# Performance work log

Measured on AMD Instinct MI355X. Metric: run time of the kernel, lower is better.

Reference implementation:

```python
import jax, jax.numpy as jnp
import numpy as np
from jax import lax

N_NEURONS = 2500
K = 50
T = 60
F = 5
H = 128
GROUP_SIZES = [800, 700, 600, 400]  # support_resistance, trend, pattern, volume
GID = jnp.asarray(np.repeat(np.arange(4), GROUP_SIZES))  # [N] specialty id per neuron
_BOUNDS = np.cumsum([0] + GROUP_SIZES)


def _lstm_layer(x, w_ih, w_hh, b_ih, b_hh):
    # x: [B,T,in]; PyTorch gate order i,f,g,o in the 4H weight rows
    B = x.shape[0]
    Hd = w_hh.shape[1]
    def step(carry, xt):
        h, c = carry
        g = xt @ w_ih.T + h @ w_hh.T + b_ih + b_hh
        i, f, gg, o = jnp.split(g, 4, axis=-1)
        c = jax.nn.sigmoid(f) * c + jax.nn.sigmoid(i) * jnp.tanh(gg)
        h = jax.nn.sigmoid(o) * jnp.tanh(c)
        return (h, c), h
    init = (jnp.zeros((B, Hd), x.dtype), jnp.zeros((B, Hd), x.dtype))
    (h, _), ys = lax.scan(step, init, jnp.swapaxes(x, 0, 1))
    return jnp.swapaxes(ys, 0, 1), h


def _forward(x, w_ih0, w_hh0, b_ih0, b_hh0, w_ih1, w_hh1, b_ih1, b_hh1,
             pw1, pb1, pw2, pb2, conn_w, sens, thr,
             iw1, ib1, iw2, ib2, iw3, ib3,
             hw_trend, hb_trend, hw_pat, hb_pat, hw_key, hb_key,
             hw_vol, hb_vol, hw_conf, hb_conf, conn_idx):
    seq, _ = _lstm_layer(x, w_ih0, w_hh0, b_ih0, b_hh0)
    _, h2 = _lstm_layer(seq, w_ih1, w_hh1, b_ih1, b_hh1)  # hidden[-1]: [B,H]
    # feature_projection: Linear->ReLU->Linear->Tanh
    base = jnp.tanh(jax.nn.relu(h2 @ pw1.T + pb1) @ pw2.T + pb2)  # [B,32]
    # broadcast base features to a per-neuron activation vector [B,N]
    reps = -(-N_NEURONS // base.shape[1])
    all_act = jnp.tile(base, (1, reps))[:, :N_NEURONS]
    # batched sparse gather + per-neuron weighted sum
    gathered = all_act[:, conn_idx]                       # [B,N,K]
    z = jnp.einsum('bnk,nk->bn', gathered, conn_w) * sens  # [B,N]
    # specialty-conditioned activation
    a = jnp.where(GID == 0, jax.nn.sigmoid(z - thr),
        jnp.where(GID == 1, jnp.tanh(z),
        jnp.where(GID == 2, jax.nn.relu(z - thr), jax.nn.sigmoid(z))))
    # integrator (dropout is eval-mode no-op)
    integ = jnp.tanh(jax.nn.relu(jax.nn.relu(a @ iw1.T + ib1) @ iw2.T + ib2) @ iw3.T + ib3)
    trend = integ @ hw_trend.T + hb_trend      # [B,3]
    pat = integ @ hw_pat.T + hb_pat            # [B,6]
    key_l = integ @ hw_key.T + hb_key          # [B,4]
    vol = integ @ hw_vol.T + hb_vol            # [B,1]
    conf = integ @ hw_conf.T + hb_conf         # [B,1]
    overall = jax.nn.sigmoid(conf)             # [B,1]
    means = jnp.stack([a[:, _BOUNDS[i]:_BOUNDS[i + 1]].mean(axis=1) for i in range(4)], axis=1)
    return jnp.concatenate([trend, pat, key_l, vol, conf, overall, means], axis=1)  # [B,20]


def setup_inputs() -> dict:
    key = jax.random.key(0)
    ks = iter(jax.random.split(key, 64))
    def rn(shape, s=0.05):
        return jax.random.normal(next(ks), shape, jnp.float32) * s
    B = 1024
    return {
        'x': jax.random.normal(next(ks), (B, T, F), jnp.float32),
        'conn_idx': jax.random.randint(next(ks), (N_NEURONS, K), 0, N_NEURONS, jnp.int32),
        'w_ih0': rn((4 * H, F)), 'w_hh0': rn((4 * H, H)),
        'b_ih0': rn((4 * H,), 0.01), 'b_hh0': rn((4 * H,), 0.01),
        'w_ih1': rn((4 * H, H)), 'w_hh1': rn((4 * H, H)),
        'b_ih1': rn((4 * H,), 0.01), 'b_hh1': rn((4 * H,), 0.01),
        'pw1': rn((64, H)), 'pb1': rn((64,), 0.01),
        'pw2': rn((32, 64)), 'pb2': rn((32,), 0.01),
        'conn_w': rn((N_NEURONS, K), 0.1),
        'sens': rn((N_NEURONS,), 0.1) + 1.0,
        'thr': rn((N_NEURONS,), 0.1) + 0.6,
        'iw1': rn((256, N_NEURONS), 0.01), 'ib1': rn((256,), 0.01),
        'iw2': rn((64, 256)), 'ib2': rn((64,), 0.01),
        'iw3': rn((32, 64)), 'ib3': rn((32,), 0.01),
        'hw_trend': rn((3, 32)), 'hb_trend': rn((3,), 0.01),
        'hw_pat': rn((6, 32)), 'hb_pat': rn((6,), 0.01),
        'hw_key': rn((4, 32)), 'hb_key': rn((4,), 0.01),
        'hw_vol': rn((1, 32)), 'hb_vol': rn((1,), 0.01),
        'hw_conf': rn((1, 32)), 'hb_conf': rn((1,), 0.01),
    }


def reference(x, conn_idx, w_ih0, w_hh0, b_ih0, b_hh0, w_ih1, w_hh1, b_ih1, b_hh1,
              pw1, pb1, pw2, pb2, conn_w, sens, thr,
              iw1, ib1, iw2, ib2, iw3, ib3,
              hw_trend, hb_trend, hw_pat, hb_pat, hw_key, hb_key,
              hw_vol, hb_vol, hw_conf, hb_conf):
    return _forward(x, w_ih0, w_hh0, b_ih0, b_hh0, w_ih1, w_hh1, b_ih1, b_hh1,
                    pw1, pb1, pw2, pb2, conn_w, sens, thr,
                    iw1, ib1, iw2, ib2, iw3, ib3,
                    hw_trend, hb_trend, hw_pat, hb_pat, hw_key, hb_key,
                    hw_vol, hb_vol, hw_conf, hb_conf, conn_idx)
```

## Files before the change

### kernel.cpp

```cpp
#include <hip/hip_runtime.h>
#include <hip/hip_bf16.h>
#include <math.h>

#define DEV __device__ __forceinline__

typedef short short8 __attribute__((ext_vector_type(8)));
typedef float f32x4  __attribute__((ext_vector_type(4)));

DEV float sigf(float x)   { return 1.0f / (1.0f + __expf(-x)); }
DEV float tanhft(float x) { return 1.0f - 2.0f / (__expf(2.0f * x) + 1.0f); }

DEV unsigned short f2bf(float f) {
    unsigned int u = __float_as_uint(f);
    unsigned int r = (u + 0x7FFFu + ((u >> 16) & 1u)) >> 16;
    return (unsigned short)r;
}
DEV float bf2f(unsigned short u) {
    return __uint_as_float(((unsigned int)u) << 16);
}

DEV void bar_lds() {
    asm volatile("s_waitcnt lgkmcnt(0)" ::: "memory");
    __builtin_amdgcn_s_barrier();
}

__global__ __launch_bounds__(256) void prep_kernel(
    const float* __restrict__ w_hh0, const float* __restrict__ w_ih1,
    const float* __restrict__ w_hh1,
    const float* __restrict__ b_ih0, const float* __restrict__ b_hh0,
    const float* __restrict__ b_ih1, const float* __restrict__ b_hh1,
    unsigned short* __restrict__ whh0h, unsigned short* __restrict__ wih1h,
    unsigned short* __restrict__ whh1h,
    float* __restrict__ bias0, float* __restrict__ bias1)
{
    int i = blockIdx.x * 256 + threadIdx.x;
    if (i < 65536) {
        whh0h[i] = f2bf(w_hh0[i]);
        wih1h[i] = f2bf(w_ih1[i]);
        whh1h[i] = f2bf(w_hh1[i]);
    } else if (i < 66048) {
        int c = i - 65536;
        bias0[c] = b_ih0[c] + b_hh0[c];
        bias1[c] = b_ih1[c] + b_hh1[c];
    }
}

__global__ __launch_bounds__(256) void prep_iw1_kernel(
    const float* __restrict__ iw1, unsigned short* __restrict__ iw1b)
{
    int i = blockIdx.x * 256 + threadIdx.x;
    if (i < 256 * 2528) {
        int row = i / 2528, k = i - row * 2528;
        iw1b[i] = (k < 2500) ? f2bf(iw1[row * 2500 + k]) : (unsigned short)0;
    }
}

__global__ __launch_bounds__(512, 2) void lstm_kernel(
    const float* __restrict__ x,
    const unsigned short* __restrict__ whh0,
    const unsigned short* __restrict__ wih1,
    const unsigned short* __restrict__ whh1,
    const float* __restrict__ wih0,
    const float* __restrict__ bias0, const float* __restrict__ bias1,
    float* __restrict__ h2out)
{
    __shared__ __align__(16) float          xs[4][304];
    __shared__ __align__(16) unsigned short h0s[2][16][136];
    __shared__ __align__(16) unsigned short h1s[2][16][136];
    __shared__ __align__(16) float          wsc[8][4][16][4];
    __shared__ float wih0s[2560];

    const int tid = threadIdx.x;
    const int b0  = blockIdx.x * 4;
    const int l15 = tid & 15;
    const int q   = (tid >> 4) & 3;
    const int w   = tid >> 6;
    const int j   = w * 16 + l15;
    const int q8  = q * 8;

    for (int i = tid; i < 1200; i += 512) {
        int m = i / 300, kk = i - m * 300;
        xs[m][kk] = x[(b0 + m) * 300 + kk];
    }
    for (int i = tid; i < 2560; i += 512) wih0s[i] = wih0[i];
    for (int i = tid; i < 2176; i += 512) {
        ((unsigned int*)h0s)[i] = 0u;
        ((unsigned int*)h1s)[i] = 0u;
    }

    float ub0[4], ub1[4];
#pragma unroll
    for (int g = 0; g < 4; ++g) {
        ub0[g] = bias0[g * 128 + j];
        ub1[g] = bias1[g * 128 + j];
    }

    short8 bh0[4][4], b1i[4][4];
#pragma unroll
    for (int g = 0; g < 4; ++g)
#pragma unroll
        for (int kc = 0; kc < 4; ++kc) {
            int off = (g * 128 + j) * 128 + kc * 32 + q8;
            bh0[g][kc] = *(const short8*)(whh0 + off);
            b1i[g][kc] = *(const short8*)(wih1 + off);
        }

    float c0 = 0.f, c1 = 0.f, hl = 0.f;
    __syncthreads();

    const unsigned short* wsb = whh1 + j * 128 + q8;

    for (int t = 0; t < 60; ++t) {
        const int p = t & 1;

        short8 wsv[4][4];
#pragma unroll
        for (int g = 0; g < 4; ++g) {
            wsv[g][0] = *(const short8*)(wsb + g * 16384);
            wsv[g][1] = *(const short8*)(wsb + g * 16384 + 32);
        }

        f32x4 acc[4];
#pragma unroll
        for (int g = 0; g < 4; ++g) acc[g] = (f32x4){0.f, 0.f, 0.f, 0.f};
        short8 af[4];
#pragma unroll
        for (int kc = 0; kc < 4; ++kc)
            af[kc] = *(const short8*)&h0s[p][l15][kc * 32 + q8];
#pragma unroll
        for (int kc = 0; kc < 4; ++kc)
#pragma unroll
            for (int g = 0; g < 4; ++g)
                acc[g] = __builtin_amdgcn_mfma_f32_16x16x32_bf16(af[kc], bh0[g][kc], acc[g], 0, 0, 0);

#pragma unroll
        for (int g = 0; g < 4; ++g) {
            wsv[g][2] = *(const short8*)(wsb + g * 16384 + 64);
            wsv[g][3] = *(const short8*)(wsb + g * 16384 + 96);
        }

        if (q == 0) {
#pragma unroll
            for (int g = 0; g < 4; ++g)
                *(f32x4*)&wsc[w][g][l15][0] = acc[g];
        }
        {
            const float* xr = &xs[q][t * 5];
            float x0 = xr[0], x1 = xr[1], x2 = xr[2], x3 = xr[3], x4 = xr[4];
            float gv[4];
#pragma unroll
            for (int g = 0; g < 4; ++g) {
                const float* wr = &wih0s[(g * 128 + j) * 5];
                float s = wsc[w][g][l15][q] + ub0[g];
                s = fmaf(x0, wr[0], s);
                s = fmaf(x1, wr[1], s);
                s = fmaf(x2, wr[2], s);
                s = fmaf(x3, wr[3], s);
                gv[g] = fmaf(x4, wr[4], s);
            }
            c0 = sigf(gv[1]) * c0 + sigf(gv[0]) * tanhft(gv[2]);
            float h = sigf(gv[3]) * tanhft(c0);
            h0s[1 - p][q][j] = f2bf(h);
        }

        bar_lds();

#pragma unroll
        for (int g = 0; g < 4; ++g) acc[g] = (f32x4){0.f, 0.f, 0.f, 0.f};
#pragma unroll
        for (int kc = 0; kc < 4; ++kc)
            af[kc] = *(const short8*)&h0s[1 - p][l15][kc * 32 + q8];
#pragma unroll
        for (int kc = 0; kc < 4; ++kc)
#pragma unroll
            for (int g = 0; g < 4; ++g)
                acc[g] = __builtin_amdgcn_mfma_f32_16x16x32_bf16(af[kc], b1i[g][kc], acc[g], 0, 0, 0);
#pragma unroll
        for (int kc = 0; kc < 4; ++kc)
            af[kc] = *(const short8*)&h1s[p][l15][kc * 32 + q8];
#pragma unroll
        for (int kc = 0; kc < 4; ++kc)
#pragma unroll
            for (int g = 0; g < 4; ++g)
                acc[g] = __builtin_amdgcn_mfma_f32_16x16x32_bf16(af[kc], wsv[g][kc], acc[g], 0, 0, 0);

        if (q == 0) {
#pragma unroll
            for (int g = 0; g < 4; ++g)
                *(f32x4*)&wsc[w][g][l15][0] = acc[g];
        }
        {
            float gv[4];
#pragma unroll
            for (int g = 0; g < 4; ++g)
                gv[g] = wsc[w][g][l15][q] + ub1[g];
            c1 = sigf(gv[1]) * c1 + sigf(gv[0]) * tanhft(gv[2]);
            float h = sigf(gv[3]) * tanhft(c1);
            h1s[1 - p][q][j] = f2bf(h);
            hl = h;
        }
    }

    h2out[(b0 + q) * 128 + j] = hl;
}

__global__ __launch_bounds__(256) void phase2_kernel(
    const float* __restrict__ h2, const float* __restrict__ pw1,
    const float* __restrict__ pb1, const float* __restrict__ pw2,
    const float* __restrict__ pb2, float* __restrict__ base)
{
    __shared__ float pw1s[64 * 129];
    __shared__ float pw2s[32 * 65];
    __shared__ float hs[4][128];
    __shared__ float p1s[4][64];

    const int tid = threadIdx.x;
    const int b0  = blockIdx.x * 4;

    for (int i = tid; i < 8192; i += 256) {
        int u = i >> 7, k = i & 127;
        pw1s[u * 129 + k] = pw1[i];
    }
    for (int i = tid; i < 2048; i += 256) {
        int u = i >> 6, k = i & 63;
        pw2s[u * 65 + k] = pw2[i];
    }
    for (int i = tid; i < 512; i += 256)
        hs[i >> 7][i & 127] = h2[b0 * 128 + i];
    __syncthreads();

    {
        const int r = tid >> 6, u = tid & 63;
        float acc = pb1[u];
        const float* wr = &pw1s[u * 129];
        const float* hr = &hs[r][0];
#pragma unroll 4
        for (int k = 0; k < 128; ++k) acc = fmaf(hr[k], wr[k], acc);
        p1s[r][u] = fmaxf(acc, 0.f);
    }
    __syncthreads();

    if (tid < 128) {
        const int r = tid >> 5, u2 = tid & 31;
        float a2 = pb2[u2];
        const float* wr = &pw2s[u2 * 65];
        const float* pr = &p1s[r][0];
#pragma unroll 4
        for (int k = 0; k < 64; ++k) a2 = fmaf(pr[k], wr[k], a2);
        base[(b0 + r) * 32 + u2] = tanhft(a2);
    }
}

__global__ __launch_bounds__(128) void weff_kernel(
    const int* __restrict__ conn_idx, const float* __restrict__ conn_w,
    float* __restrict__ weffT)
{
    __shared__ float s[128 * 33];
    int tid = threadIdx.x;
    int n = blockIdx.x * 128 + tid;
    float* sr = &s[tid * 33];
#pragma unroll
    for (int j = 0; j < 32; ++j) sr[j] = 0.f;
    if (n < 2500) {
        for (int k = 0; k < 50; ++k) {
            int idx = conn_idx[n * 50 + k];
            sr[idx & 31] += conn_w[n * 50 + k];
        }
        for (int j = 0; j < 32; ++j) weffT[j * 2500 + n] = sr[j];
    }
}

__global__ __launch_bounds__(256) void za_kernel(
    const float* __restrict__ base, const float* __restrict__ weffT,
    const float* __restrict__ sens, const float* __restrict__ thr,
    unsigned short* __restrict__ amat)
{
    __shared__ float bs[16][32];
    int tid = threadIdx.x;
    int bb = blockIdx.x / 10, nb = blockIdx.x % 10;
    int n = nb * 256 + tid;
    bool nv = n < 2500;
    bool pv = n < 2528;
    int nn = nv ? n : 0;
    for (int i = tid; i < 512; i += 256) bs[i >> 5][i & 31] = base[bb * 512 + i];
    __syncthreads();
    float w[32];
#pragma unroll
    for (int j = 0; j < 32; ++j) w[j] = weffT[j * 2500 + nn];
    float sn = sens[nn], tn = thr[nn];
    int g = (n < 800) ? 0 : (n < 1500) ? 1 : (n < 2100) ? 2 : 3;
#pragma unroll 2
    for (int r = 0; r < 16; ++r) {
        float z = 0.f;
#pragma unroll
        for (int j = 0; j < 32; ++j) z = fmaf(bs[r][j], w[j], z);
        z *= sn;
        float av;
        if (g == 0)      av = sigf(z - tn);
        else if (g == 1) av = tanhft(z);
        else if (g == 2) av = fmaxf(z - tn, 0.f);
        else             av = sigf(z);
        if (nv)      amat[(bb * 16 + r) * 2528 + n] = f2bf(av);
        else if (pv) amat[(bb * 16 + r) * 2528 + n] = 0;
    }
}

__global__ __launch_bounds__(128) void gemm_iw1_kernel(
    const unsigned short* __restrict__ ab, const unsigned short* __restrict__ wb,
    const float* __restrict__ ib1, float* __restrict__ t1)
{
    const int tid = threadIdx.x;
    const int wv  = tid >> 6;
    const int l15 = tid & 15, q = (tid >> 4) & 3, q8 = q * 8;
    const int row0 = blockIdx.y * 32 + wv * 16;
    const int col0 = blockIdx.x * 32;

    const unsigned short* A = ab + (row0 + l15) * 2528 + q8;
    const unsigned short* B = wb + (col0 + l15) * 2528 + q8;

    short8 a = *(const short8*)A;
    short8 b[2];
#pragma unroll
    for (int nt = 0; nt < 2; ++nt) b[nt] = *(const short8*)(B + nt * 16 * 2528);

    f32x4 acc[2];
#pragma unroll
    for (int nt = 0; nt < 2; ++nt) acc[nt] = (f32x4){0.f, 0.f, 0.f, 0.f};

    for (int c = 0; c < 79; ++c) {
        int cn = (c < 78) ? c + 1 : 78;
        short8 an = *(const short8*)(A + cn * 32);
        short8 bn[2];
#pragma unroll
        for (int nt = 0; nt < 2; ++nt)
            bn[nt] = *(const short8*)(B + nt * 16 * 2528 + cn * 32);
#pragma unroll
        for (int nt = 0; nt < 2; ++nt)
            acc[nt] = __builtin_amdgcn_mfma_f32_16x16x32_bf16(a, b[nt], acc[nt], 0, 0, 0);
        a = an;
#pragma unroll
        for (int nt = 0; nt < 2; ++nt) b[nt] = bn[nt];
    }

#pragma unroll
    for (int nt = 0; nt < 2; ++nt) {
        int n = col0 + nt * 16 + l15;
        float bias = ib1[n];
#pragma unroll
        for (int i = 0; i < 4; ++i) {
            int row = row0 + q * 4 + i;
            t1[row * 256 + n] = fmaxf(acc[nt][i] + bias, 0.f);
        }
    }
}

__global__ __launch_bounds__(256) void final_kernel(
    const float* __restrict__ t1, const float* __restrict__ iw2,
    const float* __restrict__ ib2, const float* __restrict__ iw3,
    const float* __restrict__ ib3,
    const float* __restrict__ hw_trend, const float* __restrict__ hb_trend,
    const float* __restrict__ hw_pat,   const float* __restrict__ hb_pat,
    const float* __restrict__ hw_key,   const float* __restrict__ hb_key,
    const float* __restrict__ hw_vol,   const float* __restrict__ hb_vol,
    const float* __restrict__ hw_conf,  const float* __restrict__ hb_conf,
    float* __restrict__ out)
{
    __shared__ float iw2s[64 * 257];
    __shared__ float iw3s[32 * 65];
    __shared__ float t1s[4][256];
    __shared__ float t2s[4][64];
    __shared__ float igs[4][32];

    const int tid = threadIdx.x;
    const int b0  = blockIdx.x * 4;

    for (int i = tid; i < 16384; i += 256) {
        int u = i >> 8, k = i & 255;
        iw2s[u * 257 + k] = iw2[i];
    }
    for (int i = tid; i < 2048; i += 256) {
        int u = i >> 6, k = i & 63;
        iw3s[u * 65 + k] = iw3[i];
    }
    for (int i = tid; i < 1024; i += 256)
        t1s[i >> 8][i & 255] = t1[b0 * 256 + i];
    __syncthreads();

    {
        const int r = tid >> 6, u = tid & 63;
        float acc = ib2[u];
        const float* wr = &iw2s[u * 257];
        const float* tr = &t1s[r][0];
#pragma unroll 4
        for (int k = 0; k < 256; ++k) acc = fmaf(tr[k], wr[k], acc);
        t2s[r][u] = fmaxf(acc, 0.f);
    }
    __syncthreads();

    if (tid < 128) {
        const int r = tid >> 5, u2 = tid & 31;
        float a2 = ib3[u2];
        const float* wr = &iw3s[u2 * 65];
        const float* tr = &t2s[r][0];
#pragma unroll 4
        for (int k = 0; k < 64; ++k) a2 = fmaf(tr[k], wr[k], a2);
        igs[r][u2] = tanhft(a2);
    }
    __syncthreads();

    if (tid < 60) {
        const int r = tid / 15, t15 = tid % 15;
        const int b = b0 + r;
        const float* w; const float* bb; int j, off;
        if (t15 < 3)        { w = hw_trend; bb = hb_trend; j = t15;     off = 0; }
        else if (t15 < 9)   { w = hw_pat;   bb = hb_pat;   j = t15 - 3; off = 3; }
        else if (t15 < 13)  { w = hw_key;   bb = hb_key;   j = t15 - 9; off = 9; }
        else if (t15 == 13) { w = hw_vol;   bb = hb_vol;   j = 0;       off = 13; }
        else                { w = hw_conf;  bb = hb_conf;  j = 0;       off = 14; }
        float a3 = bb[j];
#pragma unroll
        for (int k = 0; k < 32; ++k) a3 = fmaf(igs[r][k], w[j * 32 + k], a3);
        out[b * 20 + off + j] = a3;
        if (t15 == 14) out[b * 20 + 15] = sigf(a3);
    }
}

__global__ __launch_bounds__(256) void means_kernel(
    const unsigned short* __restrict__ amat, float* __restrict__ out)
{
    __shared__ float red[16];
    int b = blockIdx.x, tid = threadIdx.x;
    float parts[4] = {0.f, 0.f, 0.f, 0.f};
    for (int n0 = tid * 8; n0 < 2500; n0 += 2048) {
        short8 v = *(const short8*)(amat + b * 2528 + n0);
#pragma unroll
        for (int e = 0; e < 8; ++e) {
            int n = n0 + e;
            float f = bf2f((unsigned short)v[e]);
            if (n < 800)       parts[0] += f;
            else if (n < 1500) parts[1] += f;
            else if (n < 2100) parts[2] += f;
            else               parts[3] += f;
        }
    }
    int lane = tid & 63, wv = tid >> 6;
#pragma unroll
    for (int g = 0; g < 4; ++g) {
        float v = parts[g];
        for (int s = 32; s > 0; s >>= 1) v += __shfl_down(v, s, 64);
        if (lane == 0) red[wv * 4 + g] = v;
    }
    __syncthreads();
    if (tid < 4) {
        float s = red[tid] + red[4 + tid] + red[8 + tid] + red[12 + tid];
        float invg = (tid == 0) ? (1.f / 800.f) : (tid == 1) ? (1.f / 700.f)
                   : (tid == 2) ? (1.f / 600.f) : (1.f / 400.f);
        out[b * 20 + 16 + tid] = s * invg;
    }
}

extern "C" void kernel_launch(void* const* d_in, const int* in_sizes, int n_in,
                              void* d_out, int out_size, void* d_ws, size_t ws_size,
                              hipStream_t stream)
{
    const float* x        = (const float*)d_in[0];
    const int*   conn_idx = (const int*)  d_in[1];
    const float* w_ih0    = (const float*)d_in[2];
    const float* w_hh0    = (const float*)d_in[3];
    const float* b_ih0    = (const float*)d_in[4];
    const float* b_hh0    = (const float*)d_in[5];
    const float* w_ih1    = (const float*)d_in[6];
    const float* w_hh1    = (const float*)d_in[7];
    const float* b_ih1    = (const float*)d_in[8];
    const float* b_hh1    = (const float*)d_in[9];
    const float* pw1      = (const float*)d_in[10];
    const float* pb1      = (const float*)d_in[11];
    const float* pw2      = (const float*)d_in[12];
    const float* pb2      = (const float*)d_in[13];
    const float* conn_w   = (const float*)d_in[14];
    const float* sens     = (const float*)d_in[15];
    const float* thr      = (const float*)d_in[16];
    const float* iw1      = (const float*)d_in[17];
    const float* ib1      = (const float*)d_in[18];
    const float* iw2      = (const float*)d_in[19];
    const float* ib2      = (const float*)d_in[20];
    const float* iw3      = (const float*)d_in[21];
    const float* ib3      = (const float*)d_in[22];
    const float* hw_trend = (const float*)d_in[23];
    const float* hb_trend = (const float*)d_in[24];
    const float* hw_pat   = (const float*)d_in[25];
    const float* hb_pat   = (const float*)d_in[26];
    const float* hw_key   = (const float*)d_in[27];
    const float* hb_key   = (const float*)d_in[28];
    const float* hw_vol   = (const float*)d_in[29];
    const float* hb_vol   = (const float*)d_in[30];
    const float* hw_conf  = (const float*)d_in[31];
    const float* hb_conf  = (const float*)d_in[32];
    float* out = (float*)d_out;
    float* ws  = (float*)d_ws;

    unsigned short* whh0h = (unsigned short*)(ws);
    unsigned short* wih1h = (unsigned short*)(ws + 32768);
    unsigned short* whh1h = (unsigned short*)(ws + 65536);
    float* bias0  = ws + 98304;
    float* bias1  = ws + 98816;
    float* h2     = ws + 99328;
    float* base_  = ws + 230400;
    float* weffT  = ws + 263168;
    float* t1     = ws + 343168;
    unsigned short* iw1b   = (unsigned short*)(ws + 605312);
    unsigned short* amatbf = (unsigned short*)(ws + 928896);

    prep_kernel<<<258, 256, 0, stream>>>(w_hh0, w_ih1, w_hh1,
                                         b_ih0, b_hh0, b_ih1, b_hh1,
                                         whh0h, wih1h, whh1h, bias0, bias1);
    prep_iw1_kernel<<<2528, 256, 0, stream>>>(iw1, iw1b);
    lstm_kernel<<<256, 512, 0, stream>>>(x, whh0h, wih1h, whh1h, w_ih0,
                                         bias0, bias1, h2);
    phase2_kernel<<<256, 256, 0, stream>>>(h2, pw1, pb1, pw2, pb2, base_);
    weff_kernel<<<20, 128, 0, stream>>>(conn_idx, conn_w, weffT);
    za_kernel<<<640, 256, 0, stream>>>(base_, weffT, sens, thr, amatbf);
    gemm_iw1_kernel<<<dim3(8, 32), 128, 0, stream>>>(amatbf, iw1b, ib1, t1);
    final_kernel<<<256, 256, 0, stream>>>(t1, iw2, ib2, iw3, ib3,
                                          hw_trend, hb_trend, hw_pat, hb_pat,
                                          hw_key, hb_key, hw_vol, hb_vol,
                                          hw_conf, hb_conf, out);
    means_kernel<<<1024, 256, 0, stream>>>(amatbf, out);
}
```

Measured before the change: 294.9 us.

## Fuse prep kernels, projection into LSTM, means into final; deepen GEMM prefetch

Merges the two weight-prep kernels into one launch and folds the feature-projection MLP into the tail of the LSTM kernel, which removes the h2 round trip through global memory. The per-group mean computation moves into final_kernel, and weff_kernel now stages conn_idx/conn_w through LDS with coalesced loads. The iw1 GEMM gets a 4-deep register prefetch pipeline. Together these cut kernel launches and latency stalls, but the LSTM kernel gains about 42KB of extra shared memory, which may reduce its occupancy.

```diff
diff --git a/kernel.cpp b/kernel.cpp
--- a/kernel.cpp
+++ b/kernel.cpp
@@ -24,34 +24,35 @@
     __builtin_amdgcn_s_barrier();
 }
 
-__global__ __launch_bounds__(256) void prep_kernel(
+__global__ __launch_bounds__(256) void prep_all_kernel(
     const float* __restrict__ w_hh0, const float* __restrict__ w_ih1,
     const float* __restrict__ w_hh1,
     const float* __restrict__ b_ih0, const float* __restrict__ b_hh0,
     const float* __restrict__ b_ih1, const float* __restrict__ b_hh1,
+    const float* __restrict__ iw1,
     unsigned short* __restrict__ whh0h, unsigned short* __restrict__ wih1h,
     unsigned short* __restrict__ whh1h,
-    float* __restrict__ bias0, float* __restrict__ bias1)
-{
-    int i = blockIdx.x * 256 + threadIdx.x;
-    if (i < 65536) {
-        whh0h[i] = f2bf(w_hh0[i]);
-        wih1h[i] = f2bf(w_ih1[i]);
-        whh1h[i] = f2bf(w_hh1[i]);
-    } else if (i < 66048) {
-        int c = i - 65536;
-        bias0[c] = b_ih0[c] + b_hh0[c];
-        bias1[c] = b_ih1[c] + b_hh1[c];
-    }
-}
-
-__global__ __launch_bounds__(256) void prep_iw1_kernel(
-    const float* __restrict__ iw1, unsigned short* __restrict__ iw1b)
-{
-    int i = blockIdx.x * 256 + threadIdx.x;
-    if (i < 256 * 2528) {
-        int row = i / 2528, k = i - row * 2528;
-        iw1b[i] = (k < 2500) ? f2bf(iw1[row * 2500 + k]) : (unsigned short)0;
+    float* __restrict__ bias0, float* __restrict__ bias1,
+    unsigned short* __restrict__ iw1b)
+{
+    int blk = blockIdx.x;
+    if (blk < 258) {
+        int i = blk * 256 + threadIdx.x;
+        if (i < 65536) {
+            whh0h[i] = f2bf(w_hh0[i]);
+            wih1h[i] = f2bf(w_ih1[i]);
+            whh1h[i] = f2bf(w_hh1[i]);
+        } else if (i < 66048) {
+            int c = i - 65536;
+            bias0[c] = b_ih0[c] + b_hh0[c];
+            bias1[c] = b_ih1[c] + b_hh1[c];
+        }
+    } else {
+        int i = (blk - 258) * 256 + threadIdx.x;
+        if (i < 256 * 2528) {
+            int row = i / 2528, k = i - row * 2528;
+            iw1b[i] = (k < 2500) ? f2bf(iw1[row * 2500 + k]) : (unsigned short)0;
+        }
     }
 }
 
@@ -62,13 +63,18 @@
     const unsigned short* __restrict__ whh1,
     const float* __restrict__ wih0,
     const float* __restrict__ bias0, const float* __restrict__ bias1,
-    float* __restrict__ h2out)
+    const float* __restrict__ pw1, const float* __restrict__ pb1,
+    const float* __restrict__ pw2, const float* __restrict__ pb2,
+    float* __restrict__ base)
 {
     __shared__ __align__(16) float          xs[4][304];
     __shared__ __align__(16) unsigned short h0s[2][16][136];
     __shared__ __align__(16) unsigned short h1s[2][16][136];
     __shared__ __align__(16) float          wsc[8][4][16][4];
     __shared__ float wih0s[2560];
+    __shared__ float pw1s[64 * 129];
+    __shared__ float pw2s[32 * 65];
+    __shared__ float p1l[256];
 
     const int tid = threadIdx.x;
     const int b0  = blockIdx.x * 4;
@@ -201,50 +207,29 @@
         }
     }
 
-    h2out[(b0 + q) * 128 + j] = hl;
-}
-
-__global__ __launch_bounds__(256) void phase2_kernel(
-    const float* __restrict__ h2, const float* __restrict__ pw1,
-    const float* __restrict__ pb1, const float* __restrict__ pw2,
-    const float* __restrict__ pb2, float* __restrict__ base)
-{
-    __shared__ float pw1s[64 * 129];
-    __shared__ float pw2s[32 * 65];
-    __shared__ float hs[4][128];
-    __shared__ float p1s[4][64];
-
-    const int tid = threadIdx.x;
-    const int b0  = blockIdx.x * 4;
-
-    for (int i = tid; i < 8192; i += 256) {
-        int u = i >> 7, k = i & 127;
-        pw1s[u * 129 + k] = pw1[i];
-    }
-    for (int i = tid; i < 2048; i += 256) {
-        int u = i >> 6, k = i & 63;
-        pw2s[u * 65 + k] = pw2[i];
-    }
-    for (int i = tid; i < 512; i += 256)
-        hs[i >> 7][i & 127] = h2[b0 * 128 + i];
-    __syncthreads();
-
-    {
+    for (int i = tid; i < 8192; i += 512)
+        pw1s[(i >> 7) * 129 + (i & 127)] = pw1[i];
+    for (int i = tid; i < 2048; i += 512)
+        pw2s[(i >> 6) * 65 + (i & 63)] = pw2[i];
+    bar_lds();
+    float* h2l = (float*)wsc;
+    h2l[q * 128 + j] = hl;
+    bar_lds();
+    if (tid < 256) {
         const int r = tid >> 6, u = tid & 63;
         float acc = pb1[u];
         const float* wr = &pw1s[u * 129];
-        const float* hr = &hs[r][0];
+        const float* hr = &h2l[r * 128];
 #pragma unroll 4
         for (int k = 0; k < 128; ++k) acc = fmaf(hr[k], wr[k], acc);
-        p1s[r][u] = fmaxf(acc, 0.f);
-    }
-    __syncthreads();
-
+        p1l[r * 64 + u] = fmaxf(acc, 0.f);
+    }
+    bar_lds();
     if (tid < 128) {
         const int r = tid >> 5, u2 = tid & 31;
         float a2 = pb2[u2];
         const float* wr = &pw2s[u2 * 65];
-        const float* pr = &p1s[r][0];
+        const float* pr = &p1l[r * 64];
 #pragma unroll 4
         for (int k = 0; k < 64; ++k) a2 = fmaf(pr[k], wr[k], a2);
         base[(b0 + r) * 32 + u2] = tanhft(a2);
@@ -255,18 +240,29 @@
     const int* __restrict__ conn_idx, const float* __restrict__ conn_w,
     float* __restrict__ weffT)
 {
+    __shared__ int   idxp[128 * 51];
+    __shared__ float wp[128 * 51];
     __shared__ float s[128 * 33];
-    int tid = threadIdx.x;
-    int n = blockIdx.x * 128 + tid;
+    const int tid = threadIdx.x;
+    const int nb  = blockIdx.x * 128;
+    const int gbase = nb * 50;
+    for (int i = tid; i < 6400; i += 128) {
+        int r = i / 50, c = i - r * 50;
+        bool v = (nb + r) < 2500;
+        idxp[r * 51 + c] = v ? conn_idx[gbase + i] : 0;
+        wp[r * 51 + c]   = v ? conn_w[gbase + i]   : 0.f;
+    }
     float* sr = &s[tid * 33];
 #pragma unroll
-    for (int j = 0; j < 32; ++j) sr[j] = 0.f;
+    for (int jj = 0; jj < 32; ++jj) sr[jj] = 0.f;
+    __syncthreads();
+    int n = nb + tid;
     if (n < 2500) {
         for (int k = 0; k < 50; ++k) {
-            int idx = conn_idx[n * 50 + k];
-            sr[idx & 31] += conn_w[n * 50 + k];
-        }
-        for (int j = 0; j < 32; ++j) weffT[j * 2500 + n] = sr[j];
+            int idx = idxp[tid * 51 + k];
+            sr[idx & 31] += wp[tid * 51 + k];
+        }
+        for (int jj = 0; jj < 32; ++jj) weffT[jj * 2500 + n] = sr[jj];
     }
 }
 
@@ -318,44 +314,68 @@
     const unsigned short* A = ab + (row0 + l15) * 2528 + q8;
     const unsigned short* B = wb + (col0 + l15) * 2528 + q8;
 
-    short8 a = *(const short8*)A;
-    short8 b[2];
-#pragma unroll
-    for (int nt = 0; nt < 2; ++nt) b[nt] = *(const short8*)(B + nt * 16 * 2528);
-
-    f32x4 acc[2];
-#pragma unroll
-    for (int nt = 0; nt < 2; ++nt) acc[nt] = (f32x4){0.f, 0.f, 0.f, 0.f};
-
-    for (int c = 0; c < 79; ++c) {
-        int cn = (c < 78) ? c + 1 : 78;
-        short8 an = *(const short8*)(A + cn * 32);
-        short8 bn[2];
-#pragma unroll
-        for (int nt = 0; nt < 2; ++nt)
-            bn[nt] = *(const short8*)(B + nt * 16 * 2528 + cn * 32);
-#pragma unroll
-        for (int nt = 0; nt < 2; ++nt)
-            acc[nt] = __builtin_amdgcn_mfma_f32_16x16x32_bf16(a, b[nt], acc[nt], 0, 0, 0);
-        a = an;
-#pragma unroll
-        for (int nt = 0; nt < 2; ++nt) b[nt] = bn[nt];
-    }
-
-#pragma unroll
-    for (int nt = 0; nt < 2; ++nt) {
-        int n = col0 + nt * 16 + l15;
+    short8 a[4], b0v[4], b1v[4];
+#pragma unroll
+    for (int u = 0; u < 4; ++u) {
+        a[u]   = *(const short8*)(A + u * 32);
+        b0v[u] = *(const short8*)(B + u * 32);
+        b1v[u] = *(const short8*)(B + 16 * 2528 + u * 32);
+    }
+
+    f32x4 acc0 = (f32x4){0.f, 0.f, 0.f, 0.f};
+    f32x4 acc1 = (f32x4){0.f, 0.f, 0.f, 0.f};
+
+    for (int c4 = 0; c4 < 72; c4 += 4) {
+#pragma unroll
+        for (int u = 0; u < 4; ++u) {
+            short8 av = a[u], bv0 = b0v[u], bv1 = b1v[u];
+            int cn = c4 + u + 4;
+            a[u]   = *(const short8*)(A + cn * 32);
+            b0v[u] = *(const short8*)(B + cn * 32);
+            b1v[u] = *(const short8*)(B + 16 * 2528 + cn * 32);
+            acc0 = __builtin_amdgcn_mfma_f32_16x16x32_bf16(av, bv0, acc0, 0, 0, 0);
+            acc1 = __builtin_amdgcn_mfma_f32_16x16x32_bf16(av, bv1, acc1, 0, 0, 0);
+        }
+    }
+#pragma unroll
+    for (int u = 0; u < 4; ++u) {
+        short8 av = a[u], bv0 = b0v[u], bv1 = b1v[u];
+        if (u < 3) {
+            int cn = 76 + u;
+            a[u]   = *(const short8*)(A + cn * 32);
+            b0v[u] = *(const short8*)(B + cn * 32);
+            b1v[u] = *(const short8*)(B + 16 * 2528 + cn * 32);
+        }
+        acc0 = __builtin_amdgcn_mfma_f32_16x16x32_bf16(av, bv0, acc0, 0, 0, 0);
+        acc1 = __builtin_amdgcn_mfma_f32_16x16x32_bf16(av, bv1, acc1, 0, 0, 0);
+    }
+#pragma unroll
+    for (int u = 0; u < 3; ++u) {
+        acc0 = __builtin_amdgcn_mfma_f32_16x16x32_bf16(a[u], b0v[u], acc0, 0, 0, 0);
+        acc1 = __builtin_amdgcn_mfma_f32_16x16x32_bf16(a[u], b1v[u], acc1, 0, 0, 0);
+    }
+
+    {
+        int n = col0 + l15;
         float bias = ib1[n];
 #pragma unroll
         for (int i = 0; i < 4; ++i) {
             int row = row0 + q * 4 + i;
-            t1[row * 256 + n] = fmaxf(acc[nt][i] + bias, 0.f);
+            t1[row * 256 + n] = fmaxf(acc0[i] + bias, 0.f);
+        }
+        n = col0 + 16 + l15;
+        bias = ib1[n];
+#pragma unroll
+        for (int i = 0; i < 4; ++i) {
+            int row = row0 + q * 4 + i;
+            t1[row * 256 + n] = fmaxf(acc1[i] + bias, 0.f);
         }
     }
 }
 
 __global__ __launch_bounds__(256) void final_kernel(
-    const float* __restrict__ t1, const float* __restrict__ iw2,
+    const float* __restrict__ t1, const unsigned short* __restrict__ amat,
+    const float* __restrict__ iw2,
     const float* __restrict__ ib2, const float* __restrict__ iw3,
     const float* __restrict__ ib3,
     const float* __restrict__ hw_trend, const float* __restrict__ hb_trend,
@@ -370,6 +390,7 @@
     __shared__ float t1s[4][256];
     __shared__ float t2s[4][64];
     __shared__ float igs[4][32];
+    __shared__ float mred[4][4];
 
     const int tid = threadIdx.x;
     const int b0  = blockIdx.x * 4;
@@ -384,6 +405,34 @@
     }
     for (int i = tid; i < 1024; i += 256)
         t1s[i >> 8][i & 255] = t1[b0 * 256 + i];
+
+    {
+        const int lane = tid & 63, wv4 = tid >> 6;
+        const unsigned short* arow = amat + (unsigned int)(b0 + wv4) * 2528;
+        float parts[4] = {0.f, 0.f, 0.f, 0.f};
+#pragma unroll
+        for (int s = 0; s < 5; ++s) {
+            int c = lane + 64 * s;
+            if (c < 316) {
+                short8 v = *(const short8*)(arow + c * 8);
+#pragma unroll
+                for (int e = 0; e < 8; ++e) {
+                    int n = c * 8 + e;
+                    float f = bf2f((unsigned short)v[e]);
+                    if (n < 800)       parts[0] += f;
+                    else if (n < 1500) parts[1] += f;
+                    else if (n < 2100) parts[2] += f;
+                    else               parts[3] += f;
+                }
+            }
+        }
+#pragma unroll
+        for (int g = 0; g < 4; ++g) {
+            float v = parts[g];
+            for (int s2 = 32; s2 > 0; s2 >>= 1) v += __shfl_down(v, s2, 64);
+            if (lane == 0) mred[wv4][g] = v;
+        }
+    }
     __syncthreads();
 
     {
@@ -423,39 +472,10 @@
         out[b * 20 + off + j] = a3;
         if (t15 == 14) out[b * 20 + 15] = sigf(a3);
     }
-}
-
-__global__ __launch_bounds__(256) void means_kernel(
-    const unsigned short* __restrict__ amat, float* __restrict__ out)
-{
-    __shared__ float red[16];
-    int b = blockIdx.x, tid = threadIdx.x;
-    float parts[4] = {0.f, 0.f, 0.f, 0.f};
-    for (int n0 = tid * 8; n0 < 2500; n0 += 2048) {
-        short8 v = *(const short8*)(amat + b * 2528 + n0);
-#pragma unroll
-        for (int e = 0; e < 8; ++e) {
-            int n = n0 + e;
-            float f = bf2f((unsigned short)v[e]);
-            if (n < 800)       parts[0] += f;
-            else if (n < 1500) parts[1] += f;
-            else if (n < 2100) parts[2] += f;
-            else               parts[3] += f;
-        }
-    }
-    int lane = tid & 63, wv = tid >> 6;
-#pragma unroll
-    for (int g = 0; g < 4; ++g) {
-        float v = parts[g];
-        for (int s = 32; s > 0; s >>= 1) v += __shfl_down(v, s, 64);
-        if (lane == 0) red[wv * 4 + g] = v;
-    }
-    __syncthreads();
-    if (tid < 4) {
-        float s = red[tid] + red[4 + tid] + red[8 + tid] + red[12 + tid];
-        float invg = (tid == 0) ? (1.f / 800.f) : (tid == 1) ? (1.f / 700.f)
-                   : (tid == 2) ? (1.f / 600.f) : (1.f / 400.f);
-        out[b * 20 + 16 + tid] = s * invg;
+    if (tid < 16) {
+        const int r = tid >> 2, g = tid & 3;
+        const float inv[4] = {1.f / 800.f, 1.f / 700.f, 1.f / 600.f, 1.f / 400.f};
+        out[(b0 + r) * 20 + 16 + g] = mred[r][g] * inv[g];
     }
 }
 
@@ -504,26 +524,22 @@
     unsigned short* whh1h = (unsigned short*)(ws + 65536);
     float* bias0  = ws + 98304;
     float* bias1  = ws + 98816;
-    float* h2     = ws + 99328;
     float* base_  = ws + 230400;
     float* weffT  = ws + 263168;
     float* t1     = ws + 343168;
     unsigned short* iw1b   = (unsigned short*)(ws + 605312);
     unsigned short* amatbf = (unsigned short*)(ws + 928896);
 
-    prep_kernel<<<258, 256, 0, stream>>>(w_hh0, w_ih1, w_hh1,
-                                         b_ih0, b_hh0, b_ih1, b_hh1,
-                                         whh0h, wih1h, whh1h, bias0, bias1);
-    prep_iw1_kernel<<<2528, 256, 0, stream>>>(iw1, iw1b);
+    prep_all_kernel<<<2786, 256, 0, stream>>>(w_hh0, w_ih1, w_hh1,
+                                              b_ih0, b_hh0, b_ih1, b_hh1, iw1,
+                                              whh0h, wih1h, whh1h, bias0, bias1, iw1b);
     lstm_kernel<<<256, 512, 0, stream>>>(x, whh0h, wih1h, whh1h, w_ih0,
-                                         bias0, bias1, h2);
-    phase2_kernel<<<256, 256, 0, stream>>>(h2, pw1, pb1, pw2, pb2, base_);
+                                         bias0, bias1, pw1, pb1, pw2, pb2, base_);
     weff_kernel<<<20, 128, 0, stream>>>(conn_idx, conn_w, weffT);
     za_kernel<<<640, 256, 0, stream>>>(base_, weffT, sens, thr, amatbf);
     gemm_iw1_kernel<<<dim3(8, 32), 128, 0, stream>>>(amatbf, iw1b, ib1, t1);
-    final_kernel<<<256, 256, 0, stream>>>(t1, iw2, ib2, iw3, ib3,
+    final_kernel<<<256, 256, 0, stream>>>(t1, amatbf, iw2, ib2, iw3, ib3,
                                           hw_trend, hb_trend, hw_pat, hb_pat,
                                           hw_key, hb_key, hw_vol, hb_vol,
                                           hw_conf, hb_conf, out);
-    means_kernel<<<1024, 256, 0, stream>>>(amatbf, out);
-}
+}
```

Measured after the change: 307.4 us. 4.3% more time.
